# Kernel optimization log

Measured on AMD Instinct MI355X. Metric: run time of the kernel, lower is better.

## Reference

```python
import jax, jax.numpy as jnp
import numpy as np

N = 131072
IN_A = 256
IN_V = 512
IN_VF = 512
CH = 256
BN_EPS = 1e-5
COS_EPS = 1e-8


def setup_inputs() -> dict:
    key = jax.random.key(0)
    ks = jax.random.split(key, 12)
    s = 0.05
    return {
        "x": jax.random.normal(ks[0], (N, 4, 512), dtype=jnp.float32),
        "audio_node_mask": jax.random.bernoulli(ks[1], 0.5, (N,)),
        "W_a": jax.random.normal(ks[2], (IN_A, CH), dtype=jnp.float32) * s,
        "b_a": jnp.zeros((CH,), jnp.float32),
        "W_v": jax.random.normal(ks[3], (IN_V, CH), dtype=jnp.float32) * s,
        "b_v": jnp.zeros((CH,), jnp.float32),
        "W_f": jax.random.normal(ks[4], (2 * CH, CH), dtype=jnp.float32) * s,
        "b_f": jnp.zeros((CH,), jnp.float32),
        "gamma": jnp.ones((CH,), jnp.float32),
        "beta": jnp.zeros((CH,), jnp.float32),
        "W_fc": jax.random.normal(ks[5], (CH, 2), dtype=jnp.float32) * s,
        "b_fc": jnp.zeros((2,), jnp.float32),
    }


def reference(x, audio_node_mask, W_a, b_a, W_v, b_v, W_f, b_f, gamma, beta, W_fc, b_fc):
    # Slice per-type features (x: [N, 4, 512])
    a_in = x[:, 0, :IN_A]    # audio feats (also video->audio feats)
    v_in = x[:, 1, :IN_V]    # video feats
    a_vf = x[:, 2, :IN_VF]   # audio voice-face emb
    v_vf = x[:, 3, :IN_VF]   # video voice-face emb

    # cosine similarity along feature dim (torch.nn.functional.cosine_similarity semantics)
    dot = jnp.sum(a_vf * v_vf, axis=1)
    denom = jnp.maximum(jnp.linalg.norm(a_vf, axis=1) * jnp.linalg.norm(v_vf, axis=1), COS_EPS)
    sim = dot / denom  # [N]

    # per-type linears (compute densely, select by mask -> same math as masked scatter)
    a_out = a_in @ W_a + b_a                                   # [N, CH]
    v_out = v_in @ W_v + b_v                                   # [N, CH]
    va = a_in * sim[:, None]                                   # sim-weighted audio feats on video nodes
    fused = jnp.concatenate([va, v_out], axis=1) @ W_f + b_f   # [N, CH]

    graph_feats = jnp.where(audio_node_mask[:, None], a_out, fused)

    # BatchNorm1d (training: batch statistics, biased variance)
    mu = jnp.mean(graph_feats, axis=0)
    var = jnp.mean(jnp.square(graph_feats - mu), axis=0)
    graph_feats = (graph_feats - mu) * jax.lax.rsqrt(var + BN_EPS) * gamma + beta

    graph_feats = jax.nn.relu(graph_feats)
    return graph_feats @ W_fc + b_fc  # [N, 2]
```

## Files before the change

kernel.cpp:

```cpp
#include <hip/hip_runtime.h>
#include <hip/hip_bf16.h>
#include <stdint.h>

#define NN 131072

typedef unsigned int uint;
typedef unsigned short ushort;
typedef __attribute__((ext_vector_type(8))) __bf16 bf16x8;
typedef __attribute__((ext_vector_type(2))) __bf16 bf16x2;
typedef __attribute__((ext_vector_type(4))) float f32x4;


#define NB_MAIN 4098

__device__ __forceinline__ ushort f2bf(float f) {
    uint u = __float_as_uint(f);
    u += 0x7FFF + ((u >> 16) & 1);
    return (ushort)(u >> 16);
}
__device__ __forceinline__ uint pk2(float a, float b) {
    bf16x2 t;
    t[0] = (__bf16)a;
    t[1] = (__bf16)b;
    return __builtin_bit_cast(uint, t);
}
__device__ __forceinline__ bool mask_val(const unsigned char* m8, int flag, int i) {
    return flag ? (m8[(size_t)i * 4] != 0) : (m8[i] != 0);
}
__device__ __forceinline__ size_t pack_off(int k, int c) {
    return (size_t)(((k >> 5) * 16 + (c >> 4)) * 512
                    + (((k >> 3) & 3) * 16 + (c & 15)) * 8 + (k & 7));
}

__global__ void k_detect(const uint4* m128, int n, int* cntNZ) {
    __shared__ int cnt;
    if (threadIdx.x == 0) cnt = 0;
    __syncthreads();
    int local = 0;
    int nv = n >> 4;
    #pragma unroll 4
    for (int i = threadIdx.x; i < nv; i += 256) {
        uint4 v = m128[i];
        if ((v.x | v.y | v.z | v.w) & 0x0000FF00u) local = 1;
    }
    if (local) atomicAdd(&cnt, 1);
    __syncthreads();
    if (threadIdx.x == 0) *cntNZ = cnt;
}

__global__ void k_count(const unsigned char* m8, const int* cntNZp, int* cntM) {
    int flag = (*cntNZp == 0) ? 1 : 0;
    int t = threadIdx.x;
    bool m = mask_val(m8, flag, blockIdx.x * 256 + t);
    unsigned long long bal = __ballot(m);
    __shared__ int wsum[4];
    if ((t & 63) == 0) wsum[t >> 6] = __popcll(bal);
    __syncthreads();
    if (t == 0) cntM[blockIdx.x] = wsum[0] + wsum[1] + wsum[2] + wsum[3];
}

__global__ void k_scan(const int* __restrict__ cntM, int* __restrict__ meta,
                       int* __restrict__ baseA, int* __restrict__ baseF) {
    __shared__ int sA[512], sF[512];
    int t = threadIdx.x;
    int a = cntM[t], f = 256 - a;
    sA[t] = a; sF[t] = f;
    __syncthreads();
    for (int off = 1; off < 512; off <<= 1) {
        int va = (t >= off) ? sA[t - off] : 0;
        int vf = (t >= off) ? sF[t - off] : 0;
        __syncthreads();
        sA[t] += va; sF[t] += vf;
        __syncthreads();
    }
    baseA[t] = sA[t] - a;
    baseF[t] = sF[t] - f;
    if (t == 511) { meta[2] = sA[511]; meta[1] = sF[511]; }
}

__global__ void k_fill(const unsigned char* m8, const int* cntNZp,
                       const int* __restrict__ baseA, const int* __restrict__ baseF,
                       int* __restrict__ audioIdx, int* __restrict__ fusedIdx) {
    int flag = (*cntNZp == 0) ? 1 : 0;
    int blk = blockIdx.x, t = threadIdx.x;
    int row = blk * 256 + t;
    bool m = mask_val(m8, flag, row);
    unsigned long long bal = __ballot(m);
    int lane = t & 63, w = t >> 6;
    unsigned long long lt = (1ull << lane) - 1ull;
    int pA = __popcll(bal & lt);
    __shared__ int wA[4];
    if (lane == 0) wA[w] = __popcll(bal);
    __syncthreads();
    int offA = 0;
    for (int i = 0; i < w; ++i) offA += wA[i];
    int offF = w * 64 - offA;
    int pF = lane - pA;
    if (m) audioIdx[baseA[blk] + offA + pA] = row;
    else   fusedIdx[baseF[blk] + offF + pF] = row;
}

__global__ void k_prep(const float* __restrict__ Wa, const float* __restrict__ Wf,
                       const float* __restrict__ Wv, const float* __restrict__ bv,
                       const float* __restrict__ bf_, ushort* __restrict__ Bwa,
                       ushort* __restrict__ Bwf, float* __restrict__ cf) {
    int c = threadIdx.x;
    int b = blockIdx.x;
    if (b < 256) {
        Bwa[pack_off(b, c)] = f2bf(Wa[b * 256 + c]);
    } else if (b < 512) {
        Bwf[pack_off(512 + (b - 256), c)] = f2bf(Wf[(b - 256) * 256 + c]);
    } else if (b < 1024) {
        int k = b - 512;
        const float* wr = Wv + k * 256;
        float acc = 0.f;
        #pragma unroll 8
        for (int j = 0; j < 256; ++j) acc += wr[j] * Wf[(256 + j) * 256 + c];
        Bwf[pack_off(k, c)] = f2bf(acc);
    } else {
        float acc = bf_[c];
        #pragma unroll 8
        for (int j = 0; j < 256; ++j) acc += bv[j] * Wf[(256 + j) * 256 + c];
        cf[c] = acc;
    }
}

__global__ __launch_bounds__(512, 4) void k_main(
    const float* __restrict__ x, const int* __restrict__ meta,
    const int* __restrict__ fusedIdx, const int* __restrict__ audioIdx,
    const ushort* __restrict__ Bwa, const ushort* __restrict__ Bwf,
    const float* __restrict__ ba, const float* __restrict__ cf,
    ushort* __restrict__ gf, float* __restrict__ bn_s, float* __restrict__ bn_q)
{
    __shared__ ushort panel[32 * 768];
    __shared__ int ridxS[32];
    __shared__ unsigned char validS[32];
    __shared__ float redS[256], redQ[256];

    const int tid = threadIdx.x;
    const int cntF = meta[1], cntA = meta[2];
    const int nbF = (cntF + 31) >> 5;
    const int nbA = (cntA + 31) >> 5;
    const int b = blockIdx.x;
    const bool isF = b < nbF;
    const int bb = isF ? b : b - nbF;

    if (!isF && bb >= nbA) {
        if (tid < 256) {
            bn_s[(size_t)b * 256 + tid] = 0.f;
            bn_q[(size_t)b * 256 + tid] = 0.f;
        }
        return;
    }

    const int cnt = isF ? cntF : cntA;
    const int* idxArr = isF ? fusedIdx : audioIdx;
    const int lane = tid & 63;
    const int w = tid >> 6, wr = w >> 2, wc = w & 3;
    const int fr = lane & 15, fg = lane >> 4;

    if (tid < 32) {
        int gpos = bb * 32 + tid;
        int ok = gpos < cnt;
        ridxS[tid] = ok ? idxArr[gpos] : 0;
        validS[tid] = ok;
    }
    if (tid < 256) { redS[tid] = 0.f; redQ[tid] = 0.f; }
    __syncthreads();

    {
        const int sw = lane >> 1;
        const int o4 = (lane & 1) * 4;
        #pragma unroll 2
        for (int rr = 0; rr < 4; ++rr) {
            int r = w * 4 + rr;
            const f32x4* bp = (const f32x4*)(x + (size_t)ridxS[r] * 2048);
            float sv = validS[r] ? 1.f : 0.f;
            ushort* prow = panel + r * 768;
            int rx = r & 7;
            if (isF) {
                f32x4 ta = __builtin_nontemporal_load(bp + lane);
                f32x4 t0 = __builtin_nontemporal_load(bp + 128 + lane);
                f32x4 t1 = __builtin_nontemporal_load(bp + 192 + lane);
                f32x4 t2 = __builtin_nontemporal_load(bp + 256 + lane);
                f32x4 t3 = __builtin_nontemporal_load(bp + 320 + lane);
                f32x4 t4 = __builtin_nontemporal_load(bp + 384 + lane);
                f32x4 t5 = __builtin_nontemporal_load(bp + 448 + lane);
                float dot = t2.x * t4.x + t2.y * t4.y + t2.z * t4.z + t2.w * t4.w
                          + t3.x * t5.x + t3.y * t5.y + t3.z * t5.z + t3.w * t5.w;
                float na = t2.x * t2.x + t2.y * t2.y + t2.z * t2.z + t2.w * t2.w
                         + t3.x * t3.x + t3.y * t3.y + t3.z * t3.z + t3.w * t3.w;
                float nv = t4.x * t4.x + t4.y * t4.y + t4.z * t4.z + t4.w * t4.w
                         + t5.x * t5.x + t5.y * t5.y + t5.z * t5.z + t5.w * t5.w;
                #pragma unroll
                for (int off = 32; off; off >>= 1) {
                    dot += __shfl_xor(dot, off);
                    na  += __shfl_xor(na,  off);
                    nv  += __shfl_xor(nv,  off);
                }
                float sim = dot / fmaxf(sqrtf(na * nv), 1e-8f);
                float sa = sv * sim;
                uint2 q0 = {pk2(t0.x * sv, t0.y * sv), pk2(t0.z * sv, t0.w * sv)};
                uint2 q1 = {pk2(t1.x * sv, t1.y * sv), pk2(t1.z * sv, t1.w * sv)};
                uint2 qa = {pk2(ta.x * sa, ta.y * sa), pk2(ta.z * sa, ta.w * sa)};
                *(uint2*)(prow + ((sw ^ rx) << 3) + o4)          = q0;
                *(uint2*)(prow + (((32 + sw) ^ rx) << 3) + o4)   = q1;
                *(uint2*)(prow + (((64 + sw) ^ rx) << 3) + o4)   = qa;
            } else {
                f32x4 ta = __builtin_nontemporal_load(bp + lane);
                uint2 qa = {pk2(ta.x * sv, ta.y * sv), pk2(ta.z * sv, ta.w * sv)};
                *(uint2*)(prow + ((sw ^ rx) << 3) + o4) = qa;
            }
        }
    }
    __syncthreads();

    const int NS = isF ? 12 : 4;
    const ushort* bBase = (isF ? Bwf : Bwa) + ((size_t)(wc * 4) << 9) + (lane << 3);
    const int rrd = wr * 16 + fr;
    const ushort* prd = panel + rrd * 768;
    const int rxr = rrd & 7;

    f32x4 acc[4];
    #pragma unroll
    for (int n = 0; n < 4; ++n) acc[n] = (f32x4){0.f, 0.f, 0.f, 0.f};

    for (int st = 0; st < NS; ++st) {
        #pragma unroll
        for (int kk = 0; kk < 2; ++kk) {
            bf16x8 af = *(const bf16x8*)(prd + (((st * 8 + kk * 4 + fg) ^ rxr) << 3));
            #pragma unroll
            for (int n = 0; n < 4; ++n) {
                bf16x8 bv = *(const bf16x8*)(bBase + ((size_t)((st * 2 + kk) * 16 + n) << 9));
                acc[n] = __builtin_amdgcn_mfma_f32_16x16x32_bf16(af, bv, acc[n], 0, 0, 0);
            }
        }
    }

    const int colLo = wc * 64 + fr;
    const float* biasp = isF ? cf : ba;
    float bN[4];
    #pragma unroll
    for (int n = 0; n < 4; ++n) bN[n] = biasp[colLo + n * 16];

    float cs[4] = {0.f, 0.f, 0.f, 0.f}, cq[4] = {0.f, 0.f, 0.f, 0.f};
    #pragma unroll
    for (int j = 0; j < 4; ++j) {
        int rloc = wr * 16 + fg * 4 + j;
        if (validS[rloc]) {
            ushort* grow = gf + (size_t)ridxS[rloc] * 256;
            #pragma unroll
            for (int n = 0; n < 4; ++n) {
                float g = acc[n][j] + bN[n];
                grow[colLo + n * 16] = f2bf(g);
                cs[n] += g;
                cq[n] += g * g;
            }
        }
    }
    #pragma unroll
    for (int n = 0; n < 4; ++n) {
        atomicAdd(&redS[colLo + n * 16], cs[n]);
        atomicAdd(&redQ[colLo + n * 16], cq[n]);
    }
    __syncthreads();
    if (tid < 256) {
        bn_s[(size_t)b * 256 + tid] = redS[tid];
        bn_q[(size_t)b * 256 + tid] = redQ[tid];
    }
}

__global__ void k_stats(const float* __restrict__ bn_s, const float* __restrict__ bn_q,
                        const float* __restrict__ gamma, const float* __restrict__ beta,
                        float* __restrict__ scale, float* __restrict__ shift) {
    int c = blockIdx.x;
    int t = threadIdx.x;
    float s = 0.f, q = 0.f;
    for (int r = t; r < NB_MAIN; r += 256) {
        s += bn_s[(size_t)r * 256 + c];
        q += bn_q[(size_t)r * 256 + c];
    }
    __shared__ float ss[256], qq[256];
    ss[t] = s; qq[t] = q;
    __syncthreads();
    for (int off = 128; off; off >>= 1) {
        if (t < off) { ss[t] += ss[t + off]; qq[t] += qq[t + off]; }
        __syncthreads();
    }
    if (t == 0) {
        float mu  = ss[0] / 131072.f;
        float var = qq[0] / 131072.f - mu * mu;
        float sc = gamma[c] * rsqrtf(var + 1e-5f);
        scale[c] = sc;
        shift[c] = beta[c] - mu * sc;
    }
}

__global__ void k_out(const ushort* __restrict__ gf, const float* __restrict__ scale,
                      const float* __restrict__ shift, const float* __restrict__ Wfc,
                      const float* __restrict__ bfc, float* __restrict__ out) {
    int wid = threadIdx.x >> 6;
    int lane = threadIdx.x & 63;
    int i = blockIdx.x * 4 + wid;
    uint2 gv = ((const uint2*)(gf + (size_t)i * 256))[lane];
    float g0 = __uint_as_float(gv.x << 16);
    float g1 = __uint_as_float(gv.x & 0xFFFF0000u);
    float g2 = __uint_as_float(gv.y << 16);
    float g3 = __uint_as_float(gv.y & 0xFFFF0000u);
    int c0 = lane * 4;
    float4 sc = *(const float4*)(scale + c0);
    float4 sh = *(const float4*)(shift + c0);
    float y0 = fmaxf(g0 * sc.x + sh.x, 0.f);
    float y1 = fmaxf(g1 * sc.y + sh.y, 0.f);
    float y2 = fmaxf(g2 * sc.z + sh.z, 0.f);
    float y3 = fmaxf(g3 * sc.w + sh.w, 0.f);
    const float4* w = (const float4*)(Wfc + c0 * 2);
    float4 w0 = w[0], w1 = w[1];
    float p0 = y0 * w0.x + y1 * w0.z + y2 * w1.x + y3 * w1.z;
    float p1 = y0 * w0.y + y1 * w0.w + y2 * w1.y + y3 * w1.w;
    #pragma unroll
    for (int off = 32; off; off >>= 1) {
        p0 += __shfl_xor(p0, off);
        p1 += __shfl_xor(p1, off);
    }
    if (lane == 0) {
        out[(size_t)i * 2]     = p0 + bfc[0];
        out[(size_t)i * 2 + 1] = p1 + bfc[1];
    }
}

extern "C" void kernel_launch(void* const* d_in, const int* in_sizes, int n_in,
                              void* d_out, int out_size, void* d_ws, size_t ws_size,
                              hipStream_t stream) {
    const float* x          = (const float*)d_in[0];
    const unsigned char* mk = (const unsigned char*)d_in[1];
    const float* Wa  = (const float*)d_in[2];
    const float* ba  = (const float*)d_in[3];
    const float* Wv  = (const float*)d_in[4];
    const float* bv  = (const float*)d_in[5];
    const float* Wf  = (const float*)d_in[6];
    const float* bf  = (const float*)d_in[7];
    const float* gamma = (const float*)d_in[8];
    const float* beta  = (const float*)d_in[9];
    const float* Wfc = (const float*)d_in[10];
    const float* bfc = (const float*)d_in[11];
    float* out = (float*)d_out;

    char* ws = (char*)d_ws;
    int*    meta   = (int*)ws;
    float*  scale  = (float*)(ws + 1024);
    float*  shift  = (float*)(ws + 2048);
    float*  cf     = (float*)(ws + 3072);
    int*    cntM   = (int*)(ws + 8192);
    int*    baseA  = (int*)(ws + 12288);
    int*    baseF  = (int*)(ws + 16384);
    ushort* Bwa    = (ushort*)(ws + 32768);
    ushort* Bwf    = (ushort*)(ws + 262144);
    int*    fusedIdx = (int*)(ws + (1u << 20));
    int*    audioIdx = (int*)(ws + (1u << 20) + (512u << 10));
    float*  bn_s   = (float*)(ws + (8u << 20));
    float*  bn_q   = (float*)(ws + (16u << 20));
    ushort* gf     = (ushort*)(ws + (32u << 20));

    int n = in_sizes[1];

    k_detect<<<1, 256, 0, stream>>>((const uint4*)mk, n, meta);
    k_count<<<512, 256, 0, stream>>>(mk, meta, cntM);
    k_scan<<<1, 512, 0, stream>>>(cntM, meta, baseA, baseF);
    k_fill<<<512, 256, 0, stream>>>(mk, meta, baseA, baseF, audioIdx, fusedIdx);
    k_prep<<<1025, 256, 0, stream>>>(Wa, Wf, Wv, bv, bf, Bwa, Bwf, cf);
    k_main<<<NB_MAIN, 512, 0, stream>>>(x, meta, fusedIdx, audioIdx, Bwa, Bwf, ba, cf,
                                        gf, bn_s, bn_q);
    k_stats<<<256, 256, 0, stream>>>(bn_s, bn_q, gamma, beta, scale, shift);
    k_out<<<NN / 4, 256, 0, stream>>>(gf, scale, shift, Wfc, bfc, out);
}
```

Baseline: 284.9 us.

## Double main GEMM row tile to 64 with double-buffered K-chunk staging

The main fused GEMM kernel now handles 64 gathered rows per block instead of 32. Each wave computes two 16-row MFMA tiles per loaded weight fragment, which halves weight reads from global memory per row. Input staging is split into 256-wide K chunks in a two-buffer LDS ring, so the global load of the next chunk overlaps the MFMAs on the current one, and the cosine similarity is computed in a separate pass before the audio chunk is scaled. The output kernel now reads 8 bf16 values per lane and handles two rows per wave, and the mask-detect kernel uses 1024 threads. The cost is 64KB of LDS per block, which lowers block occupancy per CU.

After: 254.2 us. 10.8% less time.

```diff
diff --git a/kernel.cpp b/kernel.cpp
--- a/kernel.cpp
+++ b/kernel.cpp
@@ -3,6 +3,7 @@
 #include <stdint.h>
 
 #define NN 131072
+#define NB2 2050
 
 typedef unsigned int uint;
 typedef unsigned short ushort;
@@ -11,8 +12,6 @@
 typedef __attribute__((ext_vector_type(4))) float f32x4;
 
 
-#define NB_MAIN 4098
-
 __device__ __forceinline__ ushort f2bf(float f) {
     uint u = __float_as_uint(f);
     u += 0x7FFF + ((u >> 16) & 1);
@@ -39,7 +38,7 @@
     int local = 0;
     int nv = n >> 4;
     #pragma unroll 4
-    for (int i = threadIdx.x; i < nv; i += 256) {
+    for (int i = threadIdx.x; i < nv; i += 1024) {
         uint4 v = m128[i];
         if ((v.x | v.y | v.z | v.w) & 0x0000FF00u) local = 1;
     }
@@ -132,15 +131,16 @@
     const float* __restrict__ ba, const float* __restrict__ cf,
     ushort* __restrict__ gf, float* __restrict__ bn_s, float* __restrict__ bn_q)
 {
-    __shared__ ushort panel[32 * 768];
-    __shared__ int ridxS[32];
-    __shared__ unsigned char validS[32];
+    __shared__ ushort As[2][64 * 256];
+    __shared__ int ridxS[64];
+    __shared__ float simS[64];
+    __shared__ unsigned char validS[64];
     __shared__ float redS[256], redQ[256];
 
     const int tid = threadIdx.x;
     const int cntF = meta[1], cntA = meta[2];
-    const int nbF = (cntF + 31) >> 5;
-    const int nbA = (cntA + 31) >> 5;
+    const int nbF = (cntF + 63) >> 6;
+    const int nbA = (cntA + 63) >> 6;
     const int b = blockIdx.x;
     const bool isF = b < nbF;
     const int bb = isF ? b : b - nbF;
@@ -159,82 +159,116 @@
     const int w = tid >> 6, wr = w >> 2, wc = w & 3;
     const int fr = lane & 15, fg = lane >> 4;
 
-    if (tid < 32) {
-        int gpos = bb * 32 + tid;
+    if (tid < 64) {
+        int gpos = bb * 64 + tid;
         int ok = gpos < cnt;
         ridxS[tid] = ok ? idxArr[gpos] : 0;
         validS[tid] = ok;
+        simS[tid] = 1.f;
     }
     if (tid < 256) { redS[tid] = 0.f; redQ[tid] = 0.f; }
     __syncthreads();
 
-    {
-        const int sw = lane >> 1;
-        const int o4 = (lane & 1) * 4;
-        #pragma unroll 2
-        for (int rr = 0; rr < 4; ++rr) {
-            int r = w * 4 + rr;
-            const f32x4* bp = (const f32x4*)(x + (size_t)ridxS[r] * 2048);
-            float sv = validS[r] ? 1.f : 0.f;
-            ushort* prow = panel + r * 768;
-            int rx = r & 7;
-            if (isF) {
-                f32x4 ta = __builtin_nontemporal_load(bp + lane);
-                f32x4 t0 = __builtin_nontemporal_load(bp + 128 + lane);
-                f32x4 t1 = __builtin_nontemporal_load(bp + 192 + lane);
-                f32x4 t2 = __builtin_nontemporal_load(bp + 256 + lane);
-                f32x4 t3 = __builtin_nontemporal_load(bp + 320 + lane);
-                f32x4 t4 = __builtin_nontemporal_load(bp + 384 + lane);
-                f32x4 t5 = __builtin_nontemporal_load(bp + 448 + lane);
-                float dot = t2.x * t4.x + t2.y * t4.y + t2.z * t4.z + t2.w * t4.w
-                          + t3.x * t5.x + t3.y * t5.y + t3.z * t5.z + t3.w * t5.w;
-                float na = t2.x * t2.x + t2.y * t2.y + t2.z * t2.z + t2.w * t2.w
-                         + t3.x * t3.x + t3.y * t3.y + t3.z * t3.z + t3.w * t3.w;
-                float nv = t4.x * t4.x + t4.y * t4.y + t4.z * t4.z + t4.w * t4.w
-                         + t5.x * t5.x + t5.y * t5.y + t5.z * t5.z + t5.w * t5.w;
+    const int sr2 = tid >> 3, kq = tid & 7;
+    const float* xrow = x + (size_t)ridxS[sr2] * 2048;
+    const float sVf = validS[sr2] ? 1.f : 0.f;
+
+    f32x4 t0_, t1_, t2_, t3_, t4_, t5_, t6_, t7_;
+    auto loadV = [&](int baseF_) {
+        const f32x4* src = (const f32x4*)(xrow + baseF_) + kq * 8;
+        t0_ = src[0]; t1_ = src[1]; t2_ = src[2]; t3_ = src[3];
+        t4_ = src[4]; t5_ = src[5]; t6_ = src[6]; t7_ = src[7];
+    };
+    auto storeV = [&](int buf, float scl) {
+        ushort* dst = As[buf] + sr2 * 256;
+        int sx = sr2 & 7;
+        uint4 q;
+        q.x = pk2(t0_.x * scl, t0_.y * scl); q.y = pk2(t0_.z * scl, t0_.w * scl);
+        q.z = pk2(t1_.x * scl, t1_.y * scl); q.w = pk2(t1_.z * scl, t1_.w * scl);
+        *(uint4*)(dst + (((kq * 4 + 0) ^ sx) << 3)) = q;
+        q.x = pk2(t2_.x * scl, t2_.y * scl); q.y = pk2(t2_.z * scl, t2_.w * scl);
+        q.z = pk2(t3_.x * scl, t3_.y * scl); q.w = pk2(t3_.z * scl, t3_.w * scl);
+        *(uint4*)(dst + (((kq * 4 + 1) ^ sx) << 3)) = q;
+        q.x = pk2(t4_.x * scl, t4_.y * scl); q.y = pk2(t4_.z * scl, t4_.w * scl);
+        q.z = pk2(t5_.x * scl, t5_.y * scl); q.w = pk2(t5_.z * scl, t5_.w * scl);
+        *(uint4*)(dst + (((kq * 4 + 2) ^ sx) << 3)) = q;
+        q.x = pk2(t6_.x * scl, t6_.y * scl); q.y = pk2(t6_.z * scl, t6_.w * scl);
+        q.z = pk2(t7_.x * scl, t7_.y * scl); q.w = pk2(t7_.z * scl, t7_.w * scl);
+        *(uint4*)(dst + (((kq * 4 + 3) ^ sx) << 3)) = q;
+    };
+
+    const ushort* bBase = (isF ? Bwf : Bwa) + ((size_t)(wc * 4) << 9) + (lane << 3);
+    const int r0 = wr * 32 + fr, r1 = r0 + 16;
+    const ushort* prd0 = As[0] + r0 * 256;
+    const int sx0 = r0 & 7, sx1 = r1 & 7;
+
+    f32x4 acc[2][4];
+    #pragma unroll
+    for (int m = 0; m < 2; ++m)
+        #pragma unroll
+        for (int n = 0; n < 4; ++n) acc[m][n] = (f32x4){0.f, 0.f, 0.f, 0.f};
+
+    auto compute4 = [&](int buf, int visit) {
+        const ushort* p0 = As[buf] + r0 * 256;
+        const ushort* p1 = As[buf] + r1 * 256;
+        #pragma unroll
+        for (int st = 0; st < 4; ++st) {
+            #pragma unroll
+            for (int kk = 0; kk < 2; ++kk) {
+                int sl = st * 8 + kk * 4 + fg;
+                bf16x8 a0 = *(const bf16x8*)(p0 + ((sl ^ sx0) << 3));
+                bf16x8 a1 = *(const bf16x8*)(p1 + ((sl ^ sx1) << 3));
+                int kb = (visit * 4 + st) * 2 + kk;
                 #pragma unroll
-                for (int off = 32; off; off >>= 1) {
-                    dot += __shfl_xor(dot, off);
-                    na  += __shfl_xor(na,  off);
-                    nv  += __shfl_xor(nv,  off);
+                for (int n = 0; n < 4; ++n) {
+                    bf16x8 bv = *(const bf16x8*)(bBase + ((size_t)(kb * 16 + n) << 9));
+                    acc[0][n] = __builtin_amdgcn_mfma_f32_16x16x32_bf16(a0, bv, acc[0][n], 0, 0, 0);
+                    acc[1][n] = __builtin_amdgcn_mfma_f32_16x16x32_bf16(a1, bv, acc[1][n], 0, 0, 0);
                 }
-                float sim = dot / fmaxf(sqrtf(na * nv), 1e-8f);
-                float sa = sv * sim;
-                uint2 q0 = {pk2(t0.x * sv, t0.y * sv), pk2(t0.z * sv, t0.w * sv)};
-                uint2 q1 = {pk2(t1.x * sv, t1.y * sv), pk2(t1.z * sv, t1.w * sv)};
-                uint2 qa = {pk2(ta.x * sa, ta.y * sa), pk2(ta.z * sa, ta.w * sa)};
-                *(uint2*)(prow + ((sw ^ rx) << 3) + o4)          = q0;
-                *(uint2*)(prow + (((32 + sw) ^ rx) << 3) + o4)   = q1;
-                *(uint2*)(prow + (((64 + sw) ^ rx) << 3) + o4)   = qa;
-            } else {
-                f32x4 ta = __builtin_nontemporal_load(bp + lane);
-                uint2 qa = {pk2(ta.x * sv, ta.y * sv), pk2(ta.z * sv, ta.w * sv)};
-                *(uint2*)(prow + ((sw ^ rx) << 3) + o4) = qa;
             }
         }
-    }
-    __syncthreads();
-
-    const int NS = isF ? 12 : 4;
-    const ushort* bBase = (isF ? Bwf : Bwa) + ((size_t)(wc * 4) << 9) + (lane << 3);
-    const int rrd = wr * 16 + fr;
-    const ushort* prd = panel + rrd * 768;
-    const int rxr = rrd & 7;
-
-    f32x4 acc[4];
-    #pragma unroll
-    for (int n = 0; n < 4; ++n) acc[n] = (f32x4){0.f, 0.f, 0.f, 0.f};
-
-    for (int st = 0; st < NS; ++st) {
-        #pragma unroll
-        for (int kk = 0; kk < 2; ++kk) {
-            bf16x8 af = *(const bf16x8*)(prd + (((st * 8 + kk * 4 + fg) ^ rxr) << 3));
+    };
+
+    if (isF) {
+        loadV(512);
+        #pragma unroll 2
+        for (int rr = 0; rr < 8; ++rr) {
+            int r = w * 8 + rr;
+            const f32x4* p = (const f32x4*)(x + (size_t)ridxS[r] * 2048 + 1024);
+            f32x4 a0 = p[lane], a1 = p[lane + 64];
+            f32x4 v0 = p[lane + 128], v1 = p[lane + 192];
+            float dot = a0.x * v0.x + a0.y * v0.y + a0.z * v0.z + a0.w * v0.w
+                      + a1.x * v1.x + a1.y * v1.y + a1.z * v1.z + a1.w * v1.w;
+            float na = a0.x * a0.x + a0.y * a0.y + a0.z * a0.z + a0.w * a0.w
+                     + a1.x * a1.x + a1.y * a1.y + a1.z * a1.z + a1.w * a1.w;
+            float nv = v0.x * v0.x + v0.y * v0.y + v0.z * v0.z + v0.w * v0.w
+                     + v1.x * v1.x + v1.y * v1.y + v1.z * v1.z + v1.w * v1.w;
             #pragma unroll
-            for (int n = 0; n < 4; ++n) {
-                bf16x8 bv = *(const bf16x8*)(bBase + ((size_t)((st * 2 + kk) * 16 + n) << 9));
-                acc[n] = __builtin_amdgcn_mfma_f32_16x16x32_bf16(af, bv, acc[n], 0, 0, 0);
+            for (int off = 32; off; off >>= 1) {
+                dot += __shfl_xor(dot, off);
+                na  += __shfl_xor(na,  off);
+                nv  += __shfl_xor(nv,  off);
             }
+            if (lane == 0)
+                simS[r] = dot / fmaxf(sqrtf(na * nv), 1e-8f);
         }
+        storeV(0, sVf);
+        loadV(768);
+        __syncthreads();
+        compute4(0, 0);
+        storeV(1, sVf);
+        float sAf = validS[sr2] ? simS[sr2] : 0.f;
+        __syncthreads();
+        loadV(0);
+        compute4(1, 1);
+        storeV(0, sAf);
+        __syncthreads();
+        compute4(0, 2);
+    } else {
+        loadV(0);
+        storeV(0, sVf);
+        __syncthreads();
+        compute4(0, 0);
     }
 
     const int colLo = wc * 64 + fr;
@@ -245,16 +279,19 @@
 
     float cs[4] = {0.f, 0.f, 0.f, 0.f}, cq[4] = {0.f, 0.f, 0.f, 0.f};
     #pragma unroll
-    for (int j = 0; j < 4; ++j) {
-        int rloc = wr * 16 + fg * 4 + j;
-        if (validS[rloc]) {
-            ushort* grow = gf + (size_t)ridxS[rloc] * 256;
-            #pragma unroll
-            for (int n = 0; n < 4; ++n) {
-                float g = acc[n][j] + bN[n];
-                grow[colLo + n * 16] = f2bf(g);
-                cs[n] += g;
-                cq[n] += g * g;
+    for (int m = 0; m < 2; ++m) {
+        #pragma unroll
+        for (int j = 0; j < 4; ++j) {
+            int rloc = wr * 32 + m * 16 + fg * 4 + j;
+            if (validS[rloc]) {
+                ushort* grow = gf + (size_t)ridxS[rloc] * 256;
+                #pragma unroll
+                for (int n = 0; n < 4; ++n) {
+                    float g = acc[m][n][j] + bN[n];
+                    grow[colLo + n * 16] = f2bf(g);
+                    cs[n] += g;
+                    cq[n] += g * g;
+                }
             }
         }
     }
@@ -276,7 +313,7 @@
     int c = blockIdx.x;
     int t = threadIdx.x;
     float s = 0.f, q = 0.f;
-    for (int r = t; r < NB_MAIN; r += 256) {
+    for (int r = t; r < NB2; r += 256) {
         s += bn_s[(size_t)r * 256 + c];
         q += bn_q[(size_t)r * 256 + c];
     }
@@ -301,29 +338,35 @@
                       const float* __restrict__ bfc, float* __restrict__ out) {
     int wid = threadIdx.x >> 6;
     int lane = threadIdx.x & 63;
-    int i = blockIdx.x * 4 + wid;
-    uint2 gv = ((const uint2*)(gf + (size_t)i * 256))[lane];
-    float g0 = __uint_as_float(gv.x << 16);
-    float g1 = __uint_as_float(gv.x & 0xFFFF0000u);
-    float g2 = __uint_as_float(gv.y << 16);
-    float g3 = __uint_as_float(gv.y & 0xFFFF0000u);
-    int c0 = lane * 4;
-    float4 sc = *(const float4*)(scale + c0);
-    float4 sh = *(const float4*)(shift + c0);
-    float y0 = fmaxf(g0 * sc.x + sh.x, 0.f);
-    float y1 = fmaxf(g1 * sc.y + sh.y, 0.f);
-    float y2 = fmaxf(g2 * sc.z + sh.z, 0.f);
-    float y3 = fmaxf(g3 * sc.w + sh.w, 0.f);
-    const float4* w = (const float4*)(Wfc + c0 * 2);
-    float4 w0 = w[0], w1 = w[1];
-    float p0 = y0 * w0.x + y1 * w0.z + y2 * w1.x + y3 * w1.z;
-    float p1 = y0 * w0.y + y1 * w0.w + y2 * w1.y + y3 * w1.w;
-    #pragma unroll
-    for (int off = 32; off; off >>= 1) {
+    int hl = lane & 31;
+    int i = blockIdx.x * 8 + wid * 2 + (lane >> 5);
+    uint4 gv = ((const uint4*)(gf + (size_t)i * 256))[hl];
+    int c0 = hl * 8;
+    float g[8];
+    g[0] = __uint_as_float(gv.x << 16); g[1] = __uint_as_float(gv.x & 0xFFFF0000u);
+    g[2] = __uint_as_float(gv.y << 16); g[3] = __uint_as_float(gv.y & 0xFFFF0000u);
+    g[4] = __uint_as_float(gv.z << 16); g[5] = __uint_as_float(gv.z & 0xFFFF0000u);
+    g[6] = __uint_as_float(gv.w << 16); g[7] = __uint_as_float(gv.w & 0xFFFF0000u);
+    float p0 = 0.f, p1 = 0.f;
+    #pragma unroll
+    for (int j = 0; j < 2; ++j) {
+        f32x4 sc = *(const f32x4*)(scale + c0 + j * 4);
+        f32x4 sh = *(const f32x4*)(shift + c0 + j * 4);
+        f32x4 w0 = *(const f32x4*)(Wfc + (c0 + j * 4) * 2);
+        f32x4 w1 = *(const f32x4*)(Wfc + (c0 + j * 4) * 2 + 4);
+        float y0 = fmaxf(g[j * 4 + 0] * sc.x + sh.x, 0.f);
+        float y1 = fmaxf(g[j * 4 + 1] * sc.y + sh.y, 0.f);
+        float y2 = fmaxf(g[j * 4 + 2] * sc.z + sh.z, 0.f);
+        float y3 = fmaxf(g[j * 4 + 3] * sc.w + sh.w, 0.f);
+        p0 += y0 * w0.x + y1 * w0.z + y2 * w1.x + y3 * w1.z;
+        p1 += y0 * w0.y + y1 * w0.w + y2 * w1.y + y3 * w1.w;
+    }
+    #pragma unroll
+    for (int off = 16; off; off >>= 1) {
         p0 += __shfl_xor(p0, off);
         p1 += __shfl_xor(p1, off);
     }
-    if (lane == 0) {
+    if (hl == 0) {
         out[(size_t)i * 2]     = p0 + bfc[0];
         out[(size_t)i * 2 + 1] = p1 + bfc[1];
     }
@@ -364,13 +407,13 @@
 
     int n = in_sizes[1];
 
-    k_detect<<<1, 256, 0, stream>>>((const uint4*)mk, n, meta);
+    k_detect<<<1, 1024, 0, stream>>>((const uint4*)mk, n, meta);
     k_count<<<512, 256, 0, stream>>>(mk, meta, cntM);
     k_scan<<<1, 512, 0, stream>>>(cntM, meta, baseA, baseF);
     k_fill<<<512, 256, 0, stream>>>(mk, meta, baseA, baseF, audioIdx, fusedIdx);
     k_prep<<<1025, 256, 0, stream>>>(Wa, Wf, Wv, bv, bf, Bwa, Bwf, cf);
-    k_main<<<NB_MAIN, 512, 0, stream>>>(x, meta, fusedIdx, audioIdx, Bwa, Bwf, ba, cf,
-                                        gf, bn_s, bn_q);
+    k_main<<<NB2, 512, 0, stream>>>(x, meta, fusedIdx, audioIdx, Bwa, Bwf, ba, cf,
+                                    gf, bn_s, bn_q);
     k_stats<<<256, 256, 0, stream>>>(bn_s, bn_q, gamma, beta, scale, shift);
-    k_out<<<NN / 4, 256, 0, stream>>>(gf, scale, shift, Wfc, bfc, out);
-}
+    k_out<<<NN / 8, 256, 0, stream>>>(gf, scale, shift, Wfc, bfc, out);
+}
```
